# Performance work log

Measured on AMD Instinct MI355X. Metric: run time of the kernel, lower is better.

## Reference

```python
import jax, jax.numpy as jnp
import numpy as np

N = 50000   # nodes
E = 600000  # edges
D = 128     # in = hidden = out channels
L = 3       # num_layers
LN_EPS = 1e-5


def setup_inputs() -> dict:
    key = jax.random.key(0)
    ks = jax.random.split(key, 4)
    x = jax.random.normal(ks[0], (N, D), dtype=jnp.float32)
    edge_index = jax.random.randint(ks[1], (2, E), 0, N, dtype=jnp.int32)
    # GCNConv linear weights (glorot-ish scale) and biases, one per layer
    Ws = jax.random.normal(ks[2], (L, D, D), dtype=jnp.float32) / np.sqrt(D)
    bs = jnp.zeros((L, D), dtype=jnp.float32)
    # LayerNorm affine params per layer
    ln_w = jnp.ones((L, D), dtype=jnp.float32)
    ln_b = jnp.zeros((L, D), dtype=jnp.float32)
    # PReLU (single shared slope per layer, torch default init 0.25)
    alphas = jnp.full((L,), 0.25, dtype=jnp.float32)
    return {"x": x, "edge_index": edge_index, "Ws": Ws, "bs": bs,
            "ln_w": ln_w, "ln_b": ln_b, "alphas": alphas}


def reference(x, edge_index, Ws, bs, ln_w, ln_b, alphas):
    # --- gcn_norm: add self-loops, symmetric D^{-1/2} (A+I) D^{-1/2} ---
    loop = jnp.arange(N, dtype=edge_index.dtype)
    src = jnp.concatenate([edge_index[0], loop])  # [E+N]
    dst = jnp.concatenate([edge_index[1], loop])  # [E+N]
    deg = jax.ops.segment_sum(jnp.ones_like(dst, dtype=x.dtype), dst,
                              num_segments=N)
    dinv = jnp.where(deg > 0, jax.lax.rsqrt(jnp.maximum(deg, 1.0)), 0.0)
    norm = (dinv[src] * dinv[dst])[:, None]  # [E+N, 1]

    h = x
    for l in range(L):
        # GCNConv: linear -> gather -> scale -> scatter-add -> bias
        h = h @ Ws[l]                                   # [N, D]
        msg = h[src] * norm                             # [E+N, D]
        h = jax.ops.segment_sum(msg, dst, num_segments=N) + bs[l]
        # LayerNorm over feature dim
        mu = jnp.mean(h, axis=-1, keepdims=True)
        var = jnp.mean((h - mu) ** 2, axis=-1, keepdims=True)
        h = (h - mu) * jax.lax.rsqrt(var + LN_EPS) * ln_w[l] + ln_b[l]
        # PReLU
        h = jnp.where(h >= 0, h, alphas[l] * h)
    return h
```

## Files before the change

kernel.cpp:

```cpp
#include <hip/hip_runtime.h>
#include <hip/hip_bf16.h>

#define NN 50000
#define EE 600000
#define DD 128
#define LL 3
#define LN_EPS 1e-5f
#define CAP 64
#define ALD 136
#define POOL 16

typedef __attribute__((ext_vector_type(8))) short short8;
typedef __attribute__((ext_vector_type(4))) float floatx4;

__device__ inline unsigned short f2bf(float f) {
    union { float f; unsigned u; } a; a.f = f;
    unsigned r = a.u + 0x7fffu + ((a.u >> 16) & 1u);
    return (unsigned short)(r >> 16);
}


__global__ void fill_kernel(const int* __restrict__ src, const int* __restrict__ dst,
                            const float* __restrict__ W, unsigned short* __restrict__ Wt,
                            int* __restrict__ cnt, int* __restrict__ csrc) {
    int i = blockIdx.x * blockDim.x + threadIdx.x;
    if (i < LL * DD * DD) {
        int l = i >> 14, n = (i >> 7) & 127, k = i & 127;
        Wt[i] = f2bf(W[(l << 14) + k * DD + n]);
    }
    if (i >= EE) return;
    int d = dst[i];
    int pos = atomicAdd(&cnt[d], 1);
    csrc[(size_t)d * CAP + pos] = src[i];
}


__global__ __launch_bounds__(256) void gemm0_kernel(const float* __restrict__ A,
                                                    const unsigned short* __restrict__ Wt,
                                                    const int* __restrict__ cnt,
                                                    unsigned short* __restrict__ Cb) {
    __shared__ unsigned short alds[32 * ALD];
    int tid = threadIdx.x;
    int lane = tid & 63;
    int w = tid >> 6;
    int rowbase = blockIdx.x * 32;

    int cbase = (w & 1) * 64;
    int nIdx = cbase + (lane & 15);
    int kq = (lane >> 4) * 8;

    {
        int r = tid >> 3;
        int k0 = (tid & 7) * 16;
        int grow = rowbase + r;
        unsigned short* dstp = &alds[r * ALD + k0];
        if (grow < NN) {
            const float* ap = &A[(size_t)grow * DD + k0];
            float4 v0 = *(const float4*)&ap[0];
            float4 v1 = *(const float4*)&ap[4];
            float4 v2 = *(const float4*)&ap[8];
            float4 v3 = *(const float4*)&ap[12];
            float fv[16] = {v0.x,v0.y,v0.z,v0.w, v1.x,v1.y,v1.z,v1.w,
                            v2.x,v2.y,v2.z,v2.w, v3.x,v3.y,v3.z,v3.w};
            unsigned short uv[16];
            #pragma unroll
            for (int q = 0; q < 16; q++) uv[q] = f2bf(fv[q]);
            *(uint4*)&dstp[0] = *(uint4*)&uv[0];
            *(uint4*)&dstp[8] = *(uint4*)&uv[8];
        } else {
            uint4 z = make_uint4(0, 0, 0, 0);
            *(uint4*)&dstp[0] = z;
            *(uint4*)&dstp[8] = z;
        }
    }
    __syncthreads();

    int rbase = (w >> 1) * 16;
    int mrow = rbase + (lane & 15);
    floatx4 acc[4] = {{0.f,0.f,0.f,0.f},{0.f,0.f,0.f,0.f},
                      {0.f,0.f,0.f,0.f},{0.f,0.f,0.f,0.f}};
    #pragma unroll
    for (int t = 0; t < 4; t++) {
        short8 a = *(const short8*)&alds[mrow * ALD + t * 32 + kq];
        #pragma unroll
        for (int j = 0; j < 4; j++) {
            short8 b = *(const short8*)&Wt[(nIdx + j * 16) * DD + t * 32 + kq];
            acc[j] = __builtin_amdgcn_mfma_f32_16x16x32_bf16(a, b, acc[j], 0, 0, 0);
        }
    }

    int gnode0 = rowbase + rbase + (lane >> 4) * 4;
    #pragma unroll
    for (int i = 0; i < 4; i++) {
        int node = gnode0 + i;
        if (node < NN) {
            float dv = rsqrtf((float)(cnt[node] + 1));
            #pragma unroll
            for (int j = 0; j < 4; j++)
                Cb[(size_t)node * DD + cbase + j * 16 + (lane & 15)] = f2bf(acc[j][i] * dv);
        }
    }
}


__device__ inline void acc_row(float* acc, uint4 t) {
    unsigned uu[4] = {t.x, t.y, t.z, t.w};
    #pragma unroll
    for (int q = 0; q < 4; q++) {
        union { unsigned x; float f; } lo, hi;
        lo.x = uu[q] << 16;
        hi.x = uu[q] & 0xffff0000u;
        acc[2 * q]     += lo.f;
        acc[2 * q + 1] += hi.f;
    }
}

__device__ inline void agg_node(const unsigned short* __restrict__ Tb,
                                const int* __restrict__ cnt, const int* __restrict__ csrc,
                                const float* bv, const float* wv, const float* cv,
                                float alpha, int node, int f8, float* yv) {
    int deg = cnt[node];
    float dv = rsqrtf((float)(deg + 1));
    const int* row = &csrc[(size_t)node * CAP];

    float acc[8] = {};
    acc_row(acc, *(const uint4*)&Tb[(size_t)node * DD + f8]);

    int k = 0;
    for (; k + 4 <= deg; k += 4) {
        int4 ss = *(const int4*)&row[k];
        uint4 t0 = *(const uint4*)&Tb[(size_t)ss.x * DD + f8];
        uint4 t1 = *(const uint4*)&Tb[(size_t)ss.y * DD + f8];
        uint4 t2 = *(const uint4*)&Tb[(size_t)ss.z * DD + f8];
        uint4 t3 = *(const uint4*)&Tb[(size_t)ss.w * DD + f8];
        acc_row(acc, t0); acc_row(acc, t1); acc_row(acc, t2); acc_row(acc, t3);
    }
    for (; k < deg; k++) {
        acc_row(acc, *(const uint4*)&Tb[(size_t)row[k] * DD + f8]);
    }

    float a[8];
    float s1 = 0.f, s2 = 0.f;
    #pragma unroll
    for (int q = 0; q < 8; q++) {
        a[q] = fmaf(acc[q], dv, bv[q]);
        s1 += a[q]; s2 += a[q] * a[q];
    }
    #pragma unroll
    for (int off = 8; off > 0; off >>= 1) {
        s1 += __shfl_xor(s1, off, 16);
        s2 += __shfl_xor(s2, off, 16);
    }
    float mu = s1 * (1.f / DD);
    float var = s2 * (1.f / DD) - mu * mu;
    float rstd = rsqrtf(var + LN_EPS);
    #pragma unroll
    for (int q = 0; q < 8; q++) {
        float y = (a[q] - mu) * rstd * wv[q] + cv[q];
        yv[q] = (y >= 0.f) ? y : alpha * y;
    }
}


__global__ __launch_bounds__(256) void aggemm_kernel(
    const unsigned short* __restrict__ Tb, const int* __restrict__ cnt,
    const int* __restrict__ csrc,
    const float* __restrict__ bias, const float* __restrict__ lnw,
    const float* __restrict__ lnb, const float* __restrict__ alphas, int layer,
    const unsigned short* __restrict__ Wt, unsigned short* __restrict__ Tout) {
    __shared__ unsigned short alds[POOL * ALD];
    int tid = threadIdx.x;
    int g = tid >> 4;
    int lane16 = tid & 15;
    int f8 = lane16 * 8;
    int nodebase = blockIdx.x * POOL;

    float4 b0 = *(const float4*)&bias[f8];
    float4 b1 = *(const float4*)&bias[f8 + 4];
    float4 w0 = *(const float4*)&lnw[f8];
    float4 w1 = *(const float4*)&lnw[f8 + 4];
    float4 c0 = *(const float4*)&lnb[f8];
    float4 c1 = *(const float4*)&lnb[f8 + 4];
    float bv[8] = {b0.x, b0.y, b0.z, b0.w, b1.x, b1.y, b1.z, b1.w};
    float wv[8] = {w0.x, w0.y, w0.z, w0.w, w1.x, w1.y, w1.z, w1.w};
    float cv[8] = {c0.x, c0.y, c0.z, c0.w, c1.x, c1.y, c1.z, c1.w};
    float alpha = alphas[layer];

    {
        int node = nodebase + g;
        float yv[8];
        agg_node(Tb, cnt, csrc, bv, wv, cv, alpha, node, f8, yv);
        unsigned short pv[8];
        #pragma unroll
        for (int q = 0; q < 8; q++) pv[q] = f2bf(yv[q]);
        *(uint4*)&alds[g * ALD + f8] = *(uint4*)&pv[0];
    }
    __syncthreads();

    int lane = tid & 63;
    int w = tid >> 6;
    int cbase = w * 32;
    int kq = (lane >> 4) * 8;
    int mrow = lane & 15;
    floatx4 acc[2] = {{0.f,0.f,0.f,0.f},{0.f,0.f,0.f,0.f}};
    #pragma unroll
    for (int t = 0; t < 4; t++) {
        short8 a = *(const short8*)&alds[mrow * ALD + t * 32 + kq];
        #pragma unroll
        for (int j = 0; j < 2; j++) {
            short8 b = *(const short8*)&Wt[(cbase + j * 16 + (lane & 15)) * DD + t * 32 + kq];
            acc[j] = __builtin_amdgcn_mfma_f32_16x16x32_bf16(a, b, acc[j], 0, 0, 0);
        }
    }
    int gnode0 = nodebase + (lane >> 4) * 4;
    #pragma unroll
    for (int i = 0; i < 4; i++) {
        int node = gnode0 + i;
        float dv = rsqrtf((float)(cnt[node] + 1));
        #pragma unroll
        for (int j = 0; j < 2; j++)
            Tout[(size_t)node * DD + cbase + j * 16 + (lane & 15)] = f2bf(acc[j][i] * dv);
    }
}


__global__ __launch_bounds__(256) void agg_final_kernel(
    const unsigned short* __restrict__ Tb, const int* __restrict__ cnt,
    const int* __restrict__ csrc,
    const float* __restrict__ bias, const float* __restrict__ lnw,
    const float* __restrict__ lnb, const float* __restrict__ alphas, int layer,
    float* __restrict__ out) {
    int g = threadIdx.x >> 4;
    int lane16 = threadIdx.x & 15;
    int f8 = lane16 * 8;
    int node = blockIdx.x * 16 + g;
    if (node >= NN) return;

    float4 b0 = *(const float4*)&bias[f8];
    float4 b1 = *(const float4*)&bias[f8 + 4];
    float4 w0 = *(const float4*)&lnw[f8];
    float4 w1 = *(const float4*)&lnw[f8 + 4];
    float4 c0 = *(const float4*)&lnb[f8];
    float4 c1 = *(const float4*)&lnb[f8 + 4];
    float bv[8] = {b0.x, b0.y, b0.z, b0.w, b1.x, b1.y, b1.z, b1.w};
    float wv[8] = {w0.x, w0.y, w0.z, w0.w, w1.x, w1.y, w1.z, w1.w};
    float cv[8] = {c0.x, c0.y, c0.z, c0.w, c1.x, c1.y, c1.z, c1.w};

    float yv[8];
    agg_node(Tb, cnt, csrc, bv, wv, cv, alphas[layer], node, f8, yv);

    float* op = &out[(size_t)node * DD + f8];
    *(float4*)&op[0] = make_float4(yv[0], yv[1], yv[2], yv[3]);
    *(float4*)&op[4] = make_float4(yv[4], yv[5], yv[6], yv[7]);
}


extern "C" void kernel_launch(void* const* d_in, const int* in_sizes, int n_in,
                              void* d_out, int out_size, void* d_ws, size_t ws_size,
                              hipStream_t stream) {
    const float* x    = (const float*)d_in[0];
    const int*   ei   = (const int*)d_in[1];
    const float* Ws   = (const float*)d_in[2];
    const float* bs   = (const float*)d_in[3];
    const float* lnw  = (const float*)d_in[4];
    const float* lnb  = (const float*)d_in[5];
    const float* alphas = (const float*)d_in[6];
    float* out = (float*)d_out;

    const int* src = ei;
    const int* dst = ei + EE;

    char* ws = (char*)d_ws;
    size_t off = 0;
    auto alloc = [&](size_t bytes) -> void* {
        void* p = ws + off;
        off = (off + bytes + 255) & ~(size_t)255;
        return p;
    };
    int* cnt  = (int*)alloc(NN * sizeof(int));
    int* csrc = (int*)alloc((size_t)NN * CAP * sizeof(int));
    unsigned short* wt    = (unsigned short*)alloc((size_t)LL * DD * DD * sizeof(unsigned short));
    unsigned short* tbufA = (unsigned short*)alloc((size_t)NN * DD * sizeof(unsigned short));
    unsigned short* tbufB = (unsigned short*)alloc((size_t)NN * DD * sizeof(unsigned short));

    hipMemsetAsync(cnt, 0, NN * sizeof(int), stream);
    fill_kernel<<<(EE + 255) / 256, 256, 0, stream>>>(src, dst, Ws, wt, cnt, csrc);

    gemm0_kernel<<<(NN + 31) / 32, 256, 0, stream>>>(x, wt, cnt, tbufA);

    const int agg_grid = NN / POOL;
    aggemm_kernel<<<agg_grid, 256, 0, stream>>>(tbufA, cnt, csrc,
                                                bs + 0 * DD, lnw + 0 * DD, lnb + 0 * DD,
                                                alphas, 0, wt + 1 * DD * DD, tbufB);
    aggemm_kernel<<<agg_grid, 256, 0, stream>>>(tbufB, cnt, csrc,
                                                bs + 1 * DD, lnw + 1 * DD, lnb + 1 * DD,
                                                alphas, 1, wt + 2 * DD * DD, tbufA);
    agg_final_kernel<<<(NN + 15) / 16, 256, 0, stream>>>(tbufA, cnt, csrc,
                                                         bs + 2 * DD, lnw + 2 * DD, lnb + 2 * DD,
                                                         alphas, 2, out);
}
```

Baseline: 243.6 us.

## Fuse CSR fill into first GEMM and move source-degree scaling into aggregation

```diff
diff --git a/kernel.cpp b/kernel.cpp
--- a/kernel.cpp
+++ b/kernel.cpp
@@ -9,6 +9,7 @@
 #define CAP 64
 #define ALD 136
 #define POOL 16
+#define G0BLK ((NN + 31) / 32)
 
 typedef __attribute__((ext_vector_type(8))) short short8;
 typedef __attribute__((ext_vector_type(4))) float floatx4;
@@ -20,31 +21,35 @@
 }
 
 
-__global__ void fill_kernel(const int* __restrict__ src, const int* __restrict__ dst,
-                            const float* __restrict__ W, unsigned short* __restrict__ Wt,
-                            int* __restrict__ cnt, int* __restrict__ csrc) {
-    int i = blockIdx.x * blockDim.x + threadIdx.x;
-    if (i < LL * DD * DD) {
+__global__ __launch_bounds__(256) void init_kernel(const float* __restrict__ W,
+                                                   unsigned short* __restrict__ Wt,
+                                                   int* __restrict__ cnt) {
+    for (int i = blockIdx.x * 256 + threadIdx.x; i < NN; i += gridDim.x * 256)
+        cnt[i] = 0;
+    for (int i = blockIdx.x * 256 + threadIdx.x; i < LL * DD * DD; i += gridDim.x * 256) {
         int l = i >> 14, n = (i >> 7) & 127, k = i & 127;
         Wt[i] = f2bf(W[(l << 14) + k * DD + n]);
     }
-    if (i >= EE) return;
-    int d = dst[i];
-    int pos = atomicAdd(&cnt[d], 1);
-    csrc[(size_t)d * CAP + pos] = src[i];
-}
-
-
-__global__ __launch_bounds__(256) void gemm0_kernel(const float* __restrict__ A,
-                                                    const unsigned short* __restrict__ Wt,
-                                                    const int* __restrict__ cnt,
-                                                    unsigned short* __restrict__ Cb) {
+}
+
+
+__global__ __launch_bounds__(256) void gemm0_fill_kernel(
+    const float* __restrict__ A, const unsigned short* __restrict__ Wt,
+    const int* __restrict__ src, const int* __restrict__ dst,
+    int* __restrict__ cnt, int* __restrict__ csrc,
+    unsigned short* __restrict__ Cb) {
     __shared__ unsigned short alds[32 * ALD];
     int tid = threadIdx.x;
+
+    for (int e = blockIdx.x * 256 + tid; e < EE; e += G0BLK * 256) {
+        int d = dst[e];
+        int pos = atomicAdd(&cnt[d], 1);
+        csrc[(size_t)d * CAP + pos] = src[e];
+    }
+
     int lane = tid & 63;
     int w = tid >> 6;
     int rowbase = blockIdx.x * 32;
-
     int cbase = (w & 1) * 64;
     int nIdx = cbase + (lane & 15);
     int kq = (lane >> 4) * 8;
@@ -94,24 +99,23 @@
     for (int i = 0; i < 4; i++) {
         int node = gnode0 + i;
         if (node < NN) {
-            float dv = rsqrtf((float)(cnt[node] + 1));
             #pragma unroll
             for (int j = 0; j < 4; j++)
-                Cb[(size_t)node * DD + cbase + j * 16 + (lane & 15)] = f2bf(acc[j][i] * dv);
+                Cb[(size_t)node * DD + cbase + j * 16 + (lane & 15)] = f2bf(acc[j][i]);
         }
     }
 }
 
 
-__device__ inline void acc_row(float* acc, uint4 t) {
+__device__ inline void acc_row_w(float* acc, uint4 t, float w) {
     unsigned uu[4] = {t.x, t.y, t.z, t.w};
     #pragma unroll
     for (int q = 0; q < 4; q++) {
         union { unsigned x; float f; } lo, hi;
         lo.x = uu[q] << 16;
         hi.x = uu[q] & 0xffff0000u;
-        acc[2 * q]     += lo.f;
-        acc[2 * q + 1] += hi.f;
+        acc[2 * q]     += w * lo.f;
+        acc[2 * q + 1] += w * hi.f;
     }
 }
 
@@ -124,19 +128,26 @@
     const int* row = &csrc[(size_t)node * CAP];
 
     float acc[8] = {};
-    acc_row(acc, *(const uint4*)&Tb[(size_t)node * DD + f8]);
+    acc_row_w(acc, *(const uint4*)&Tb[(size_t)node * DD + f8], dv);
 
     int k = 0;
     for (; k + 4 <= deg; k += 4) {
         int4 ss = *(const int4*)&row[k];
+        float w0 = rsqrtf((float)(cnt[ss.x] + 1));
+        float w1 = rsqrtf((float)(cnt[ss.y] + 1));
+        float w2 = rsqrtf((float)(cnt[ss.z] + 1));
+        float w3 = rsqrtf((float)(cnt[ss.w] + 1));
         uint4 t0 = *(const uint4*)&Tb[(size_t)ss.x * DD + f8];
         uint4 t1 = *(const uint4*)&Tb[(size_t)ss.y * DD + f8];
         uint4 t2 = *(const uint4*)&Tb[(size_t)ss.z * DD + f8];
         uint4 t3 = *(const uint4*)&Tb[(size_t)ss.w * DD + f8];
-        acc_row(acc, t0); acc_row(acc, t1); acc_row(acc, t2); acc_row(acc, t3);
+        acc_row_w(acc, t0, w0); acc_row_w(acc, t1, w1);
+        acc_row_w(acc, t2, w2); acc_row_w(acc, t3, w3);
     }
     for (; k < deg; k++) {
-        acc_row(acc, *(const uint4*)&Tb[(size_t)row[k] * DD + f8]);
+        int s = row[k];
+        float w = rsqrtf((float)(cnt[s] + 1));
+        acc_row_w(acc, *(const uint4*)&Tb[(size_t)s * DD + f8], w);
     }
 
     float a[8];
@@ -216,10 +227,9 @@
     #pragma unroll
     for (int i = 0; i < 4; i++) {
         int node = gnode0 + i;
-        float dv = rsqrtf((float)(cnt[node] + 1));
         #pragma unroll
         for (int j = 0; j < 2; j++)
-            Tout[(size_t)node * DD + cbase + j * 16 + (lane & 15)] = f2bf(acc[j][i] * dv);
+            Tout[(size_t)node * DD + cbase + j * 16 + (lane & 15)] = f2bf(acc[j][i]);
     }
 }
 
@@ -283,10 +293,8 @@
     unsigned short* tbufA = (unsigned short*)alloc((size_t)NN * DD * sizeof(unsigned short));
     unsigned short* tbufB = (unsigned short*)alloc((size_t)NN * DD * sizeof(unsigned short));
 
-    hipMemsetAsync(cnt, 0, NN * sizeof(int), stream);
-    fill_kernel<<<(EE + 255) / 256, 256, 0, stream>>>(src, dst, Ws, wt, cnt, csrc);
-
-    gemm0_kernel<<<(NN + 31) / 32, 256, 0, stream>>>(x, wt, cnt, tbufA);
+    init_kernel<<<256, 256, 0, stream>>>(Ws, wt, cnt);
+    gemm0_fill_kernel<<<G0BLK, 256, 0, stream>>>(x, wt, src, dst, cnt, csrc, tbufA);
 
     const int agg_grid = NN / POOL;
     aggemm_kernel<<<agg_grid, 256, 0, stream>>>(tbufA, cnt, csrc,
```

After: 235.8 us. -3.2%, faster.
